# Optimization experiments

Hardware: AMD Instinct MI355X
Metric: run time of the kernel (lower is better)

The kernel has to match this reference:

```python
import jax, jax.numpy as jnp
from jax import lax
import numpy as np

B, I, T, H = 128, 512, 256, 1024


def setup_inputs() -> dict:
    key = jax.random.key(0)
    k1, k2, k3, k4, k5 = jax.random.split(key, 5)
    s = 1.0 / np.sqrt(H)  # PyTorch LSTM init scale
    return {
        "x": jax.random.normal(k1, (B, I, T), jnp.float32),
        "W_ih": jax.random.uniform(k2, (4 * H, I), jnp.float32, -s, s),
        "W_hh": jax.random.uniform(k3, (4 * H, H), jnp.float32, -s, s),
        "b_ih": jax.random.uniform(k4, (4 * H,), jnp.float32, -s, s),
        "b_hh": jax.random.uniform(k5, (4 * H,), jnp.float32, -s, s),
    }


def reference(x, W_ih, W_hh, b_ih, b_hh):
    # x: [B, I, T] -> module transposes to [B, T, I]; scan over time.
    xs = jnp.transpose(x, (2, 0, 1))  # [T, B, I]
    # Precompute input projections for all timesteps (one big GEMM).
    x_proj = jnp.einsum('tbi,gi->tbg', xs, W_ih) + b_ih + b_hh  # [T, B, 4H]
    H_ = W_hh.shape[1]

    def step(carry, xp):
        h, c = carry
        gates = xp + h @ W_hh.T  # [B, 4H]
        i, f, g, o = jnp.split(gates, 4, axis=-1)  # PyTorch gate order i,f,g,o
        i = jax.nn.sigmoid(i)
        f = jax.nn.sigmoid(f)
        g = jnp.tanh(g)
        o = jax.nn.sigmoid(o)
        c = f * c + i * g
        h = o * jnp.tanh(c)
        return (h, c), None

    h0 = jnp.zeros((x.shape[0], H_), x.dtype)
    (h, _), _ = lax.scan(step, (h0, h0), x_proj)
    return h  # [B, H] == h_t.squeeze(0)
```

## Files before the change

### kernel.cpp

```cpp
#include <hip/hip_runtime.h>
#include <hip/hip_bf16.h>
#include <cstdint>
#include <cstddef>

#define B_ 128
#define I_ 512
#define T_ 256
#define H_ 1024

typedef __attribute__((ext_vector_type(8))) short short8;
typedef __attribute__((ext_vector_type(4))) float floatx4;
typedef __attribute__((ext_vector_type(16))) float floatx16;

static __device__ __forceinline__ unsigned short f2bf(float f) {
  unsigned u = __float_as_uint(f);
  u += 0x7FFFu + ((u >> 16) & 1u);
  return (unsigned short)(u >> 16);
}
static __device__ __forceinline__ short8 pack_bf8(floatx4 a, floatx4 b) {
  short8 v;
  v[0] = (short)f2bf(a[0]); v[1] = (short)f2bf(a[1]);
  v[2] = (short)f2bf(a[2]); v[3] = (short)f2bf(a[3]);
  v[4] = (short)f2bf(b[0]); v[5] = (short)f2bf(b[1]);
  v[6] = (short)f2bf(b[2]); v[7] = (short)f2bf(b[3]);
  return v;
}
static __device__ __forceinline__ floatx16 zero16() {
  return (floatx16){0.f,0.f,0.f,0.f,0.f,0.f,0.f,0.f,
                    0.f,0.f,0.f,0.f,0.f,0.f,0.f,0.f};
}

__global__ void __launch_bounds__(256) k_transpose(
    const float* __restrict__ x, unsigned short* __restrict__ xs) {
  __shared__ float tile[64][65];
  const int b  = blockIdx.x;
  const int i0 = blockIdx.y * 64;
  const int t0 = blockIdx.z * 64;
  const int tid = threadIdx.x;
  const int c = tid & 63, r4 = tid >> 6;
  const float* src = x + (size_t)b * I_ * T_ + (size_t)i0 * T_ + t0;
#pragma unroll
  for (int it = 0; it < 16; ++it) {
    const int r = it * 4 + r4;
    tile[r][c] = src[(size_t)r * T_ + c];
  }
  __syncthreads();
#pragma unroll
  for (int it = 0; it < 16; ++it) {
    const int tr = it * 4 + r4;
    xs[((size_t)(t0 + tr) * B_ + b) * I_ + i0 + c] = f2bf(tile[c][tr]);
  }
}

__global__ void __launch_bounds__(256, 1) k_lstm(
    const unsigned short* __restrict__ xs,
    const float* __restrict__ Whh,
    const float* __restrict__ Wih,
    const float* __restrict__ bih,
    const float* __restrict__ bhh,
    unsigned short* __restrict__ hring,
    float* __restrict__ out,
    unsigned int* __restrict__ flags)
{
  extern __shared__ char smem[];
  unsigned short (*hst)[32][264] = (unsigned short (*)[32][264])smem;
  float (*gx)[2][32][34] = (float (*)[2][32][34])(smem + 101376);

  const int wg = blockIdx.x, tid = threadIdx.x;
  const int lane = tid & 63, wave = tid >> 6;
  const int bt = wg & 3, jt = wg >> 2;
  const int b0 = bt * 32, j0 = jt * 16;
  const int arow = lane & 31;
  const int hi = lane >> 5;
  const int xch = wave >> 1;
  const int xoff = (wave & 1) * 128;
  const int hch = 2 + wave;
  const size_t HBUF = (size_t)B_ * H_;

  short8 whf[2][16];
  short8 wif[2][8];
#pragma unroll
  for (int g2 = 0; g2 < 2; ++g2) {
    const int gate = g2 * 2 + (arow >> 4);
    const int wcol = j0 + (arow & 15);
    const float* wrow = Whh + (size_t)(gate * H_ + wcol) * H_ + wave * 256;
#pragma unroll
    for (int kc = 0; kc < 16; ++kc) {
      floatx4 wa = *(const floatx4*)(wrow + kc * 16 + hi * 8);
      floatx4 wb = *(const floatx4*)(wrow + kc * 16 + hi * 8 + 4);
      whf[g2][kc] = pack_bf8(wa, wb);
    }
    const float* irow = Wih + (size_t)(gate * H_ + wcol) * I_ + wave * 128;
#pragma unroll
    for (int kc = 0; kc < 8; ++kc) {
      floatx4 wa = *(const floatx4*)(irow + kc * 16 + hi * 8);
      floatx4 wb = *(const floatx4*)(irow + kc * 16 + hi * 8 + 4);
      wif[g2][kc] = pack_bf8(wa, wb);
    }
  }

  const int eb = tid >> 3;
  const int ejp = tid & 7;
  float bias[4][2];
#pragma unroll
  for (int q = 0; q < 4; ++q)
#pragma unroll
    for (int jj = 0; jj < 2; ++jj)
      bias[q][jj] = bih[q * H_ + j0 + ejp * 2 + jj] + bhh[q * H_ + j0 + ejp * 2 + jj];

  const int srow = tid >> 3;
  const int sq = tid & 7;

  float c0 = 0.f, c1 = 0.f;

  for (int t = 0; t < T_; ++t) {
    const unsigned short* hin = hring + (size_t)t * HBUF;
    unsigned short* hout = hring + (size_t)((t + 1) & 255) * HBUF;
    const unsigned short* xrow = xs + ((size_t)t * B_ + b0 + srow) * I_ + sq * 8;
    const unsigned short* hrow = hin + (size_t)(b0 + srow) * H_ + sq * 8;

    short8 xv[8];
#pragma unroll
    for (int c2 = 0; c2 < 2; ++c2)
#pragma unroll
      for (int p = 0; p < 4; ++p)
        xv[c2 * 4 + p] = *(const short8*)(xrow + c2 * 256 + p * 64);
#pragma unroll
    for (int c2 = 0; c2 < 2; ++c2)
#pragma unroll
      for (int p = 0; p < 4; ++p)
        *(short8*)&hst[c2][srow][sq * 8 + p * 64] = xv[c2 * 4 + p];
    __syncthreads();

    floatx16 acc0 = zero16(), acc1 = zero16();

    if (t > 0 && wave == 0) {
      const unsigned tgt = (unsigned)t;
      for (;;) {
        unsigned v = __hip_atomic_load(&flags[(bt + 4 * lane) * 16],
                                       __ATOMIC_RELAXED, __HIP_MEMORY_SCOPE_AGENT);
        if (__ballot(v >= tgt) == ~0ull) break;
        __builtin_amdgcn_s_sleep(1);
      }
    }

#pragma unroll
    for (int kc = 0; kc < 8; ++kc) {
      short8 a = *(const short8*)&hst[xch][arow][xoff + kc * 16 + hi * 8];
      acc0 = __builtin_amdgcn_mfma_f32_32x32x16_bf16(a, wif[0][kc], acc0, 0, 0, 0);
      acc1 = __builtin_amdgcn_mfma_f32_32x32x16_bf16(a, wif[1][kc], acc1, 0, 0, 0);
    }
    __syncthreads();

    if (t > 0) {
      short8 hv8[16];
#pragma unroll
      for (int k = 0; k < 16; ++k)
        hv8[k] = *(const short8*)(hrow + (k >> 2) * 256 + (k & 3) * 64);

#pragma unroll
      for (int ch = 0; ch < 4; ++ch)
#pragma unroll
        for (int p = 0; p < 4; ++p)
          *(short8*)&hst[2 + ch][srow][sq * 8 + p * 64] = hv8[ch * 4 + p];
      __syncthreads();
#pragma unroll
      for (int kc = 0; kc < 16; ++kc) {
        short8 a = *(const short8*)&hst[hch][arow][kc * 16 + hi * 8];
        acc0 = __builtin_amdgcn_mfma_f32_32x32x16_bf16(a, whf[0][kc], acc0, 0, 0, 0);
        acc1 = __builtin_amdgcn_mfma_f32_32x32x16_bf16(a, whf[1][kc], acc1, 0, 0, 0);
      }
    }

#pragma unroll
    for (int r = 0; r < 16; ++r) {
      const int row = (r & 3) + 8 * (r >> 2) + 4 * hi;
      gx[wave][0][row][arow] = acc0[r];
      gx[wave][1][row][arow] = acc1[r];
    }
    __syncthreads();

    float2 s_i = {0.f, 0.f}, s_f = {0.f, 0.f}, s_g = {0.f, 0.f}, s_o = {0.f, 0.f};
#pragma unroll
    for (int w = 0; w < 4; ++w) {
      s_i.x += gx[w][0][eb][ejp * 2];      s_i.y += gx[w][0][eb][ejp * 2 + 1];
      s_f.x += gx[w][0][eb][16 + ejp * 2]; s_f.y += gx[w][0][eb][16 + ejp * 2 + 1];
      s_g.x += gx[w][1][eb][ejp * 2];      s_g.y += gx[w][1][eb][ejp * 2 + 1];
      s_o.x += gx[w][1][eb][16 + ejp * 2]; s_o.y += gx[w][1][eb][16 + ejp * 2 + 1];
    }
    float hv0 = 0.f, hv1 = 0.f;
#pragma unroll
    for (int jj = 0; jj < 2; ++jj) {
      float gi = (jj ? s_i.y : s_i.x) + bias[0][jj];
      float gf = (jj ? s_f.y : s_f.x) + bias[1][jj];
      float gg = (jj ? s_g.y : s_g.x) + bias[2][jj];
      float go = (jj ? s_o.y : s_o.x) + bias[3][jj];
      float si = 1.f / (1.f + __expf(-gi));
      float sf = 1.f / (1.f + __expf(-gf));
      float tg = 2.f / (1.f + __expf(-2.f * gg)) - 1.f;
      float so = 1.f / (1.f + __expf(-go));
      float& cc = jj ? c1 : c0;
      cc = sf * cc + si * tg;
      float th = 2.f / (1.f + __expf(-2.f * cc)) - 1.f;
      float hv = so * th;
      if (jj == 0) hv0 = hv; else hv1 = hv;
    }
    const unsigned hpack = (unsigned)f2bf(hv0) | ((unsigned)f2bf(hv1) << 16);
    __hip_atomic_store((unsigned*)(hout + (size_t)(b0 + eb) * H_ + j0 + ejp * 2),
                       hpack, __ATOMIC_RELAXED, __HIP_MEMORY_SCOPE_AGENT);
    if (t == T_ - 1) {
      out[(size_t)(b0 + eb) * H_ + j0 + ejp * 2 + 0] = hv0;
      out[(size_t)(b0 + eb) * H_ + j0 + ejp * 2 + 1] = hv1;
    }

    __syncthreads();
    if (tid == 0)
      __hip_atomic_store(&flags[wg * 16], (unsigned)(t + 1), __ATOMIC_RELAXED,
                         __HIP_MEMORY_SCOPE_AGENT);
  }
}

extern "C" void kernel_launch(void* const* d_in, const int* in_sizes, int n_in,
                              void* d_out, int out_size, void* d_ws, size_t ws_size,
                              hipStream_t stream) {
  (void)in_sizes; (void)n_in; (void)out_size; (void)ws_size;
  const float* x   = (const float*)d_in[0];
  const float* Wih = (const float*)d_in[1];
  const float* Whh = (const float*)d_in[2];
  const float* bih = (const float*)d_in[3];
  const float* bhh = (const float*)d_in[4];
  float* out = (float*)d_out;

  char* ws = (char*)d_ws;
  unsigned short* xs = (unsigned short*)ws;
  unsigned int*   fl = (unsigned int*)  (ws + 33554432);
  unsigned short* hring = (unsigned short*)d_in[0];

  hipMemsetAsync(fl, 0, 16384, stream);

  k_transpose<<<dim3(B_, I_ / 64, T_ / 64), 256, 0, stream>>>(x, xs);

  const int LDS_TOTAL = 136192;
  hipFuncSetAttribute((const void*)k_lstm,
                      hipFuncAttributeMaxDynamicSharedMemorySize, LDS_TOTAL);
  k_lstm<<<dim3(256), dim3(256), LDS_TOTAL, stream>>>(
      xs, Whh, Wih, bih, bhh, hring, out, fl);
}
```

Baseline: 1.132 ms.

## Per-wave flag sync, register-prefetched x fragments, double-buffered gate LDS

Restructures the recurrent LSTM loop. Each wave now polls per-wave flags and loads its own h slice into a private LDS region, removing most block-wide barriers. x fragments are prefetched straight into registers two steps ahead, replacing the LDS staging, and the gate-reduction buffer is double-buffered so only one __syncthreads remains per step. The risks are more flag polling traffic, higher register pressure from the extra x fragment arrays, and fragile hand-placed waitcnt ordering for visibility of h.

```diff
diff --git a/kernel.cpp b/kernel.cpp
--- a/kernel.cpp
+++ b/kernel.cpp
@@ -64,7 +64,7 @@
 {
   extern __shared__ char smem[];
   unsigned short (*hst)[32][264] = (unsigned short (*)[32][264])smem;
-  float (*gx)[2][32][34] = (float (*)[2][32][34])(smem + 101376);
+  float (*gx)[4][2][32][36] = (float (*)[4][2][32][36])(smem + 67584);
 
   const int wg = blockIdx.x, tid = threadIdx.x;
   const int lane = tid & 63, wave = tid >> 6;
@@ -72,9 +72,6 @@
   const int b0 = bt * 32, j0 = jt * 16;
   const int arow = lane & 31;
   const int hi = lane >> 5;
-  const int xch = wave >> 1;
-  const int xoff = (wave & 1) * 128;
-  const int hch = 2 + wave;
   const size_t HBUF = (size_t)B_ * H_;
 
   short8 whf[2][16];
@@ -108,116 +105,138 @@
     for (int jj = 0; jj < 2; ++jj)
       bias[q][jj] = bih[q * H_ + j0 + ejp * 2 + jj] + bhh[q * H_ + j0 + ejp * 2 + jj];
 
-  const int srow = tid >> 3;
-  const int sq = tid & 7;
+  const unsigned short* xfr =
+      xs + (size_t)(b0 + arow) * I_ + wave * 128 + hi * 8;
+
+  short8 xvA[8], xvB[8];
+#pragma unroll
+  for (int kc = 0; kc < 8; ++kc) {
+    xvA[kc] = *(const short8*)(xfr + kc * 16);
+    xvB[kc] = *(const short8*)(xfr + (size_t)B_ * I_ + kc * 16);
+  }
 
   float c0 = 0.f, c1 = 0.f;
 
-  for (int t = 0; t < T_; ++t) {
-    const unsigned short* hin = hring + (size_t)t * HBUF;
-    unsigned short* hout = hring + (size_t)((t + 1) & 255) * HBUF;
-    const unsigned short* xrow = xs + ((size_t)t * B_ + b0 + srow) * I_ + sq * 8;
-    const unsigned short* hrow = hin + (size_t)(b0 + srow) * H_ + sq * 8;
-
-    short8 xv[8];
-#pragma unroll
-    for (int c2 = 0; c2 < 2; ++c2)
-#pragma unroll
-      for (int p = 0; p < 4; ++p)
-        xv[c2 * 4 + p] = *(const short8*)(xrow + c2 * 256 + p * 64);
-#pragma unroll
-    for (int c2 = 0; c2 < 2; ++c2)
-#pragma unroll
-      for (int p = 0; p < 4; ++p)
-        *(short8*)&hst[c2][srow][sq * 8 + p * 64] = xv[c2 * 4 + p];
-    __syncthreads();
-
-    floatx16 acc0 = zero16(), acc1 = zero16();
-
-    if (t > 0 && wave == 0) {
-      const unsigned tgt = (unsigned)t;
-      for (;;) {
-        unsigned v = __hip_atomic_load(&flags[(bt + 4 * lane) * 16],
-                                       __ATOMIC_RELAXED, __HIP_MEMORY_SCOPE_AGENT);
-        if (__ballot(v >= tgt) == ~0ull) break;
-        __builtin_amdgcn_s_sleep(1);
-      }
-    }
-
-#pragma unroll
-    for (int kc = 0; kc < 8; ++kc) {
-      short8 a = *(const short8*)&hst[xch][arow][xoff + kc * 16 + hi * 8];
-      acc0 = __builtin_amdgcn_mfma_f32_32x32x16_bf16(a, wif[0][kc], acc0, 0, 0, 0);
-      acc1 = __builtin_amdgcn_mfma_f32_32x32x16_bf16(a, wif[1][kc], acc1, 0, 0, 0);
-    }
-    __syncthreads();
-
-    if (t > 0) {
-      short8 hv8[16];
-#pragma unroll
-      for (int k = 0; k < 16; ++k)
-        hv8[k] = *(const short8*)(hrow + (k >> 2) * 256 + (k & 3) * 64);
-
-#pragma unroll
-      for (int ch = 0; ch < 4; ++ch)
-#pragma unroll
-        for (int p = 0; p < 4; ++p)
-          *(short8*)&hst[2 + ch][srow][sq * 8 + p * 64] = hv8[ch * 4 + p];
-      __syncthreads();
-#pragma unroll
-      for (int kc = 0; kc < 16; ++kc) {
-        short8 a = *(const short8*)&hst[hch][arow][kc * 16 + hi * 8];
-        acc0 = __builtin_amdgcn_mfma_f32_32x32x16_bf16(a, whf[0][kc], acc0, 0, 0, 0);
-        acc1 = __builtin_amdgcn_mfma_f32_32x32x16_bf16(a, whf[1][kc], acc1, 0, 0, 0);
-      }
-    }
-
-#pragma unroll
-    for (int r = 0; r < 16; ++r) {
-      const int row = (r & 3) + 8 * (r >> 2) + 4 * hi;
-      gx[wave][0][row][arow] = acc0[r];
-      gx[wave][1][row][arow] = acc1[r];
-    }
-    __syncthreads();
-
-    float2 s_i = {0.f, 0.f}, s_f = {0.f, 0.f}, s_g = {0.f, 0.f}, s_o = {0.f, 0.f};
-#pragma unroll
-    for (int w = 0; w < 4; ++w) {
-      s_i.x += gx[w][0][eb][ejp * 2];      s_i.y += gx[w][0][eb][ejp * 2 + 1];
-      s_f.x += gx[w][0][eb][16 + ejp * 2]; s_f.y += gx[w][0][eb][16 + ejp * 2 + 1];
-      s_g.x += gx[w][1][eb][ejp * 2];      s_g.y += gx[w][1][eb][ejp * 2 + 1];
-      s_o.x += gx[w][1][eb][16 + ejp * 2]; s_o.y += gx[w][1][eb][16 + ejp * 2 + 1];
-    }
-    float hv0 = 0.f, hv1 = 0.f;
-#pragma unroll
-    for (int jj = 0; jj < 2; ++jj) {
-      float gi = (jj ? s_i.y : s_i.x) + bias[0][jj];
-      float gf = (jj ? s_f.y : s_f.x) + bias[1][jj];
-      float gg = (jj ? s_g.y : s_g.x) + bias[2][jj];
-      float go = (jj ? s_o.y : s_o.x) + bias[3][jj];
-      float si = 1.f / (1.f + __expf(-gi));
-      float sf = 1.f / (1.f + __expf(-gf));
-      float tg = 2.f / (1.f + __expf(-2.f * gg)) - 1.f;
-      float so = 1.f / (1.f + __expf(-go));
-      float& cc = jj ? c1 : c0;
-      cc = sf * cc + si * tg;
-      float th = 2.f / (1.f + __expf(-2.f * cc)) - 1.f;
-      float hv = so * th;
-      if (jj == 0) hv0 = hv; else hv1 = hv;
-    }
-    const unsigned hpack = (unsigned)f2bf(hv0) | ((unsigned)f2bf(hv1) << 16);
-    __hip_atomic_store((unsigned*)(hout + (size_t)(b0 + eb) * H_ + j0 + ejp * 2),
-                       hpack, __ATOMIC_RELAXED, __HIP_MEMORY_SCOPE_AGENT);
-    if (t == T_ - 1) {
-      out[(size_t)(b0 + eb) * H_ + j0 + ejp * 2 + 0] = hv0;
-      out[(size_t)(b0 + eb) * H_ + j0 + ejp * 2 + 1] = hv1;
-    }
-
-    __syncthreads();
-    if (tid == 0)
-      __hip_atomic_store(&flags[wg * 16], (unsigned)(t + 1), __ATOMIC_RELAXED,
-                         __HIP_MEMORY_SCOPE_AGENT);
-  }
+#define LSTM_STEP(T, XCUR)                                                     \
+  {                                                                            \
+    const int t = (T);                                                         \
+    floatx16 acc0 = zero16(), acc1 = zero16();                                 \
+    short8 hld[16];                                                            \
+    if (t > 0) {                                                               \
+                            \
+      const unsigned tgt = (unsigned)t;                                        \
+      const unsigned int* fp =                                                 \
+          flags + (size_t)(4 * (16 * wave + (lane >> 2)) + bt) * 16 +          \
+          (lane & 3);                                                          \
+      for (;;) {                                                               \
+        unsigned v = __hip_atomic_load(fp, __ATOMIC_RELAXED,                   \
+                                       __HIP_MEMORY_SCOPE_AGENT);              \
+        if (__ballot(v >= tgt) == ~0ull) break;                                \
+        __builtin_amdgcn_s_sleep(1);                                           \
+      }                                                                        \
+      asm volatile("" ::: "memory");                                           \
+                     \
+      const unsigned short* hbase = hring + (size_t)t * HBUF;                  \
+      _Pragma("unroll")                                                        \
+      for (int k = 0; k < 16; ++k) {                                           \
+        const int row = (k & 1) * 16 + (lane >> 2);                            \
+        const int col = (lane & 3) * 8 + (k >> 1) * 32;                        \
+        hld[k] = *(const short8*)(hbase + (size_t)(b0 + row) * H_ +            \
+                                  wave * 256 + col);                           \
+      }                                                                        \
+    }                                                                          \
+                                \
+    _Pragma("unroll")                                                          \
+    for (int kc = 0; kc < 8; ++kc) {                                           \
+      acc0 = __builtin_amdgcn_mfma_f32_32x32x16_bf16(XCUR[kc], wif[0][kc],     \
+                                                     acc0, 0, 0, 0);           \
+      acc1 = __builtin_amdgcn_mfma_f32_32x32x16_bf16(XCUR[kc], wif[1][kc],     \
+                                                     acc1, 0, 0, 0);           \
+    }                                                                          \
+    if (t > 0) {                                                               \
+            \
+      _Pragma("unroll")                                                        \
+      for (int k = 0; k < 16; ++k) {                                           \
+        const int row = (k & 1) * 16 + (lane >> 2);                            \
+        const int col = (lane & 3) * 8 + (k >> 1) * 32;                        \
+        *(short8*)&hst[wave][row][col] = hld[k];                               \
+      }                                                                        \
+      asm volatile("s_waitcnt lgkmcnt(0)" ::: "memory");                       \
+      _Pragma("unroll")                                                        \
+      for (int kc = 0; kc < 16; ++kc) {                                        \
+        short8 a = *(const short8*)&hst[wave][arow][kc * 16 + hi * 8];         \
+        acc0 = __builtin_amdgcn_mfma_f32_32x32x16_bf16(a, whf[0][kc],          \
+                                                       acc0, 0, 0, 0);         \
+        acc1 = __builtin_amdgcn_mfma_f32_32x32x16_bf16(a, whf[1][kc],          \
+                                                       acc1, 0, 0, 0);         \
+      }                                                                        \
+    }                                                                          \
+          \
+    float (*gxb)[2][32][36] = gx[t & 1];                                       \
+    _Pragma("unroll")                                                          \
+    for (int r = 0; r < 16; ++r) {                                             \
+      const int row = (r & 3) + 8 * (r >> 2) + 4 * hi;                         \
+      gxb[wave][0][row][arow] = acc0[r];                                       \
+      gxb[wave][1][row][arow] = acc1[r];                                       \
+    }                                                                          \
+    __syncthreads();          \
+           \
+    float2 s_i = {0.f, 0.f}, s_f = {0.f, 0.f};                                 \
+    float2 s_g = {0.f, 0.f}, s_o = {0.f, 0.f};                                 \
+    _Pragma("unroll")                                                          \
+    for (int w = 0; w < 4; ++w) {                                              \
+      float2 a0 = *(const float2*)&gxb[w][0][eb][ejp * 2];                     \
+      float2 a1 = *(const float2*)&gxb[w][0][eb][16 + ejp * 2];                \
+      float2 p0 = *(const float2*)&gxb[w][1][eb][ejp * 2];                     \
+      float2 p1 = *(const float2*)&gxb[w][1][eb][16 + ejp * 2];                \
+      s_i.x += a0.x; s_i.y += a0.y; s_f.x += a1.x; s_f.y += a1.y;              \
+      s_g.x += p0.x; s_g.y += p0.y; s_o.x += p1.x; s_o.y += p1.y;              \
+    }                                                                          \
+    float hv0 = 0.f, hv1 = 0.f;                                                \
+    _Pragma("unroll")                                                          \
+    for (int jj = 0; jj < 2; ++jj) {                                           \
+      float gi = (jj ? s_i.y : s_i.x) + bias[0][jj];                           \
+      float gf = (jj ? s_f.y : s_f.x) + bias[1][jj];                           \
+      float gg = (jj ? s_g.y : s_g.x) + bias[2][jj];                           \
+      float go = (jj ? s_o.y : s_o.x) + bias[3][jj];                           \
+      float si = 1.f / (1.f + __expf(-gi));                                    \
+      float sf = 1.f / (1.f + __expf(-gf));                                    \
+      float tg = 2.f / (1.f + __expf(-2.f * gg)) - 1.f;                        \
+      float so = 1.f / (1.f + __expf(-go));                                    \
+      float& cc = jj ? c1 : c0;                                                \
+      cc = sf * cc + si * tg;                                                  \
+      float th = 2.f / (1.f + __expf(-2.f * cc)) - 1.f;                        \
+      float hv = so * th;                                                      \
+      if (jj == 0) hv0 = hv; else hv1 = hv;                                    \
+    }                                                                          \
+    unsigned short* hout = hring + (size_t)((t + 1) & 255) * HBUF;             \
+    const unsigned hpack = (unsigned)f2bf(hv0) | ((unsigned)f2bf(hv1) << 16);  \
+    __hip_atomic_store(                                                        \
+        (unsigned*)(hout + (size_t)(b0 + eb) * H_ + j0 + ejp * 2), hpack,      \
+        __ATOMIC_RELAXED, __HIP_MEMORY_SCOPE_AGENT);                           \
+    if (t == T_ - 1) {                                                         \
+      out[(size_t)(b0 + eb) * H_ + j0 + ejp * 2 + 0] = hv0;                    \
+      out[(size_t)(b0 + eb) * H_ + j0 + ejp * 2 + 1] = hv1;                    \
+    }                                                                          \
+               \
+    asm volatile("s_waitcnt vmcnt(0)" ::: "memory");                           \
+    if (lane == 0)                                                             \
+      __hip_atomic_store(&flags[wg * 16 + wave], (unsigned)(t + 1),            \
+                         __ATOMIC_RELAXED, __HIP_MEMORY_SCOPE_AGENT);          \
+        \
+    if (t + 2 < T_) {                                                          \
+      const unsigned short* xp = xfr + (size_t)(t + 2) * B_ * I_;              \
+      _Pragma("unroll")                                                        \
+      for (int kc = 0; kc < 8; ++kc)                                           \
+        XCUR[kc] = *(const short8*)(xp + kc * 16);                             \
+    }                                                                          \
+  }
+
+  for (int t2 = 0; t2 < T_; t2 += 2) {
+    LSTM_STEP(t2, xvA);
+    LSTM_STEP(t2 + 1, xvB);
+  }
+#undef LSTM_STEP
 }
 
 extern "C" void kernel_launch(void* const* d_in, const int* in_sizes, int n_in,
@@ -240,7 +259,7 @@
 
   k_transpose<<<dim3(B_, I_ / 64, T_ / 64), 256, 0, stream>>>(x, xs);
 
-  const int LDS_TOTAL = 136192;
+  const int LDS_TOTAL = 141312;
   hipFuncSetAttribute((const void*)k_lstm,
                       hipFuncAttributeMaxDynamicSharedMemorySize, LDS_TOTAL);
   k_lstm<<<dim3(256), dim3(256), LDS_TOTAL, stream>>>(
```

Measured after the change: 1.545 ms. 1.37x slower.
